# Kernel tuning notes

Measured on AMD Instinct MI355X. Metric: run time of the kernel, lower is better.

Reference implementation:

```python
import jax, jax.numpy as jnp
import numpy as np

H = 25  # fixed state size per module source
N_STEPS = 10


def _lstm_cell(x, h, c, W_ih, W_hh, b_ih, b_hh):
    # PyTorch LSTMCell: gates ordered i, f, g, o
    gates = x @ W_ih.T + b_ih + h @ W_hh.T + b_hh  # [B, 4H]
    i, f, g, o = jnp.split(gates, 4, axis=-1)
    c_new = jax.nn.sigmoid(f) * c + jax.nn.sigmoid(i) * jnp.tanh(g)
    h_new = jax.nn.sigmoid(o) * jnp.tanh(c_new)
    return h_new, c_new


def setup_inputs() -> dict:
    key = jax.random.key(0)
    ks = jax.random.split(key, 11)
    B, A = 131072, 18

    def u(k, shape, fan_in, fan_out):
        bound = np.sqrt(6.0 / (fan_in + fan_out)).astype(np.float32)
        return jax.random.uniform(k, shape, jnp.float32, -bound, bound)

    state = jax.random.normal(ks[0], (B, H), jnp.float32)
    # LSTMCell weights [4H, H]; biases zeroed per module init
    W_ih_enc = u(ks[1], (4 * H, H), H, 4 * H)
    W_hh_enc = u(ks[2], (4 * H, H), H, 4 * H)
    b_ih_enc = jnp.zeros((4 * H,), jnp.float32)
    b_hh_enc = jnp.zeros((4 * H,), jnp.float32)
    W_ih_dec = u(ks[3], (4 * H, H), H, 4 * H)
    W_hh_dec = u(ks[4], (4 * H, H), H, 4 * H)
    b_ih_dec = jnp.zeros((4 * H,), jnp.float32)
    b_hh_dec = jnp.zeros((4 * H,), jnp.float32)
    # actor head: norm_col_init std=0.01, bias 0
    w = jax.random.normal(ks[5], (A, H), jnp.float32)
    W_act = w * (0.01 / jnp.sqrt((w ** 2).sum(1, keepdims=True)))
    b_act = jnp.zeros((A,), jnp.float32)
    return {
        "state_repr_input": state,
        "W_ih_enc": W_ih_enc, "W_hh_enc": W_hh_enc, "b_ih_enc": b_ih_enc, "b_hh_enc": b_hh_enc,
        "W_ih_dec": W_ih_dec, "W_hh_dec": W_hh_dec, "b_ih_dec": b_ih_dec, "b_hh_dec": b_hh_dec,
        "W_act": W_act, "b_act": b_act,
    }


def reference(state_repr_input, W_ih_enc, W_hh_enc, b_ih_enc, b_hh_enc,
              W_ih_dec, W_hh_dec, b_ih_dec, b_hh_dec, W_act, b_act):
    B = state_repr_input.shape[0]
    zeros = jnp.zeros_like(state_repr_input)

    # Encoder: input to each step is previous hx (first step: state)
    def enc_step(carry, _):
        inp, h, c = carry
        h, c = _lstm_cell(inp, h, c, W_ih_enc, W_hh_enc, b_ih_enc, b_hh_enc)
        return (h, h, c), h

    (_, _, _), enc_hs = jax.lax.scan(enc_step, (state_repr_input, zeros, zeros), None, length=N_STEPS)
    # enc_hs: [10, B, 25]

    # Decoder: consumes encoder outputs in order
    def dec_step(carry, x):
        h, c = carry
        h, c = _lstm_cell(x, h, c, W_ih_dec, W_hh_dec, b_ih_dec, b_hh_dec)
        return (h, c), None

    (hx_dec, _), _ = jax.lax.scan(dec_step, (zeros, zeros), enc_hs)

    actor_lang = hx_dec @ W_act.T + b_act  # [B, A]
    return actor_lang, enc_hs
```

## Files before the change

kernel.cpp:

```cpp
#include <hip/hip_runtime.h>


#define HH 25
#define NSTEP 10
#define AOUT 18
#define WPB 8
#define BLK (WPB * 64)
#define NFRG 26
#define FPAD 40
#define LOG2E 1.44269504088896340736f

typedef __attribute__((ext_vector_type(8))) short short8;
typedef __attribute__((ext_vector_type(4))) float f32x4;

__device__ __forceinline__ short f2bf(float x) {
    unsigned u = __float_as_uint(x);
    u += 0x7fffu + ((u >> 16) & 1u);
    return (short)(u >> 16);
}
__device__ __forceinline__ unsigned cvtpk(float lo, float hi) {
    unsigned r;
    asm("v_cvt_pk_bf16_f32 %0, %1, %2" : "=v"(r) : "v"(lo), "v"(hi));
    return r;
}
#if __has_builtin(__builtin_amdgcn_exp2f)
#define EXP2(x) __builtin_amdgcn_exp2f(x)
#else
#define EXP2(x) exp2f(x)
#endif
#define RCP(x) __builtin_amdgcn_rcpf(x)
#define MFMA16(a, b, c) __builtin_amdgcn_mfma_f32_16x16x32_bf16((a), (b), (c), 0, 0, 0)

__global__ __launch_bounds__(BLK, 4)
void langnn_mfma16(const float* __restrict__ state,
                   const float* __restrict__ Wih_e, const float* __restrict__ Whh_e,
                   const float* __restrict__ bih_e, const float* __restrict__ bhh_e,
                   const float* __restrict__ Wih_d, const float* __restrict__ Whh_d,
                   const float* __restrict__ bih_d, const float* __restrict__ bhh_d,
                   const float* __restrict__ Wact, const float* __restrict__ bact,
                   float* __restrict__ out, int B)
{
    __shared__ __align__(16) short sFrag[NFRG][64][8];
    __shared__ __align__(16) short sH[2][WPB][16][FPAD];

    const int tid  = threadIdx.x;
    const int lane = tid & 63;
    const int w    = tid >> 6;
    const int r    = lane & 15;
    const int g    = lane >> 4;

    for (int i = tid; i < NFRG * 64; i += BLK) {
        const int idx = i >> 6, l = i & 63;
        const int lj = l & 15, lg = l >> 4;
        const float *W1 = nullptr, *W2 = nullptr, *B1 = nullptr, *B2 = nullptr;
        int gt = 0, jt, jmax = HH;
        if (idx < 8)       { gt = idx >> 1;        jt = idx & 1; W1 = Wih_e; W2 = Whh_e; B1 = bih_e; B2 = bhh_e; }
        else if (idx < 16) { gt = (idx - 8) >> 1;  jt = idx & 1; W1 = Wih_d; B1 = bih_d; B2 = bhh_d; }
        else if (idx < 24) { gt = (idx - 16) >> 1; jt = idx & 1; W1 = Whh_d; }
        else               { jt = idx - 24;        W1 = Wact;    B1 = bact;  jmax = AOUT; }
        const bool actor = (idx >= 24);
        const float sc = actor ? 1.f : (gt == 2 ? 2.f * LOG2E : -LOG2E);
        const int col = jt * 16 + lj;
        const int nrow = actor ? col : gt * HH + col;
        for (int e = 0; e < 8; ++e) {
            const int k = lg * 8 + e;
            float v = 0.f;
            if (col < jmax) {
                if (k < HH) {
                    v = W1[nrow * HH + k];
                    if (W2) v += W2[nrow * HH + k];
                    v *= sc;
                } else if (k == HH && B1) {
                    v = B1[nrow];
                    if (B2) v += B2[nrow];
                    v *= sc;
                }
            }
            sFrag[idx][l][e] = f2bf(v);
        }
    }
    {
        short* W0 = &sH[1][0][0][0];
        for (int i = tid; i < 8 * 64; i += BLK) {
            const int idx = i >> 6, l = i & 63;
            const int lj = l & 15, lg = l >> 4;
            const int gt = idx >> 1, jt = idx & 1;
            const float sc = (gt == 2 ? 2.f * LOG2E : -LOG2E);
            const int col = jt * 16 + lj;
            const int nrow = gt * HH + col;
            for (int e = 0; e < 8; ++e) {
                const int k = lg * 8 + e;
                float v = 0.f;
                if (col < HH) {
                    if (k < HH)       v = Wih_e[nrow * HH + k] * sc;
                    else if (k == HH) v = (bih_e[nrow] + bhh_e[nrow]) * sc;
                }
                W0[(size_t)idx * 512 + l * 8 + e] = f2bf(v);
            }
        }
    }
    {
        int* z = (int*)&sH[0][0][0][0];
        for (int i = tid; i < WPB * 16 * (FPAD / 2); i += BLK)
            z[i] = ((i % (FPAD / 2)) == 12) ? 0x3F800000 : 0;
    }
    __syncthreads();

    const int b0 = (blockIdx.x * WPB + w) * 16;
    float* pe = out + (size_t)B * AOUT + (size_t)(b0 + g * 4) * HH + r;

    float ce[2][4], cd[2][4];
    #pragma unroll
    for (int jt = 0; jt < 2; ++jt)
        #pragma unroll
        for (int q = 0; q < 4; ++q) { ce[jt][q] = 0.f; cd[jt][q] = 0.f; }

    short8 aE, aD;
    {
        const float* sp0 = state + (size_t)(b0 + r) * HH;
        #pragma unroll
        for (int e = 0; e < 8; ++e) {
            const int k = g * 8 + e;
            aE[e] = (k < HH) ? f2bf(sp0[k]) : (k == HH ? (short)0x3F80 : (short)0);
            aD[e] = (k == HH) ? (short)0x3F80 : (short)0;
        }
    }

    auto encCell = [&](const short (*FB)[64][8]) {
        #pragma unroll
        for (int jt = 0; jt < 2; ++jt) {
            f32x4 acc[4];
            #pragma unroll
            for (int gt = 0; gt < 4; ++gt) {
                short8 Bf = *(const short8*)&FB[gt * 2 + jt][lane][0];
                f32x4 z; z[0] = z[1] = z[2] = z[3] = 0.f;
                acc[gt] = MFMA16(aE, Bf, z);
            }
            float hv[4];
            #pragma unroll
            for (int q = 0; q < 4; ++q) {
                float Ei = EXP2(acc[0][q]);
                float Ef = EXP2(acc[1][q]);
                float Eg = EXP2(acc[2][q]);
                float Eo = EXP2(acc[3][q]);
                float Pf = 1.f + Ef;
                float Pig = (1.f + Ei) * (1.f + Eg);
                float c = fmaf(ce[jt][q], Pig, (Eg - 1.f) * Pf) * RCP(Pf * Pig);
                ce[jt][q] = c;
                float Ec = EXP2(2.f * LOG2E * c);
                float Pc = 1.f + Ec;
                hv[q] = (Pc - 2.f) * RCP(Pc * (1.f + Eo));
            }
            if (jt == 0 || r < 9) {
                float* p = pe + jt * 16;
                p[0] = hv[0]; p[HH] = hv[1]; p[2 * HH] = hv[2]; p[3 * HH] = hv[3];
                unsigned p01 = cvtpk(hv[0], hv[1]), p23 = cvtpk(hv[2], hv[3]);
                short* sp = &sH[0][w][g * 4][jt * 16 + r];
                sp[0]        = (short)p01;
                sp[FPAD]     = (short)(p01 >> 16);
                sp[2 * FPAD] = (short)p23;
                sp[3 * FPAD] = (short)(p23 >> 16);
            }
        }
        aE = *(const short8*)&sH[0][w][r][g * 8];
        pe += (size_t)B * HH;
    };

    auto decCell = [&]() {
        #pragma unroll
        for (int jt = 0; jt < 2; ++jt) {
            f32x4 acc[4];
            #pragma unroll
            for (int gt = 0; gt < 4; ++gt) {
                short8 Bx = *(const short8*)&sFrag[8 + gt * 2 + jt][lane][0];
                short8 Bh = *(const short8*)&sFrag[16 + gt * 2 + jt][lane][0];
                f32x4 z; z[0] = z[1] = z[2] = z[3] = 0.f;
                acc[gt] = MFMA16(aD, Bh, MFMA16(aE, Bx, z));
            }
            float hv[4];
            #pragma unroll
            for (int q = 0; q < 4; ++q) {
                float Ei = EXP2(acc[0][q]);
                float Ef = EXP2(acc[1][q]);
                float Eg = EXP2(acc[2][q]);
                float Eo = EXP2(acc[3][q]);
                float Pf = 1.f + Ef;
                float Pig = (1.f + Ei) * (1.f + Eg);
                float c = fmaf(cd[jt][q], Pig, (Eg - 1.f) * Pf) * RCP(Pf * Pig);
                cd[jt][q] = c;
                float Ec = EXP2(2.f * LOG2E * c);
                float Pc = 1.f + Ec;
                hv[q] = (Pc - 2.f) * RCP(Pc * (1.f + Eo));
            }
            if (jt == 0 || r < 9) {
                unsigned p01 = cvtpk(hv[0], hv[1]), p23 = cvtpk(hv[2], hv[3]);
                short* sp = &sH[1][w][g * 4][jt * 16 + r];
                sp[0]        = (short)p01;
                sp[FPAD]     = (short)(p01 >> 16);
                sp[2 * FPAD] = (short)p23;
                sp[3 * FPAD] = (short)(p23 >> 16);
            }
        }
        aD = *(const short8*)&sH[1][w][r][g * 8];
    };

    encCell((const short (*)[64][8])&sH[1][0][0][0]);
    __syncthreads();
    {
        int* z = (int*)&sH[1][w][0][0];
        for (int i = lane; i < 16 * (FPAD / 2); i += 64)
            z[i] = ((i % (FPAD / 2)) == 12) ? 0x3F800000 : 0;
    }
    decCell();
    #pragma unroll 1
    for (int t = 1; t < NSTEP; ++t) {
        encCell(sFrag);
        decCell();
    }

    #pragma unroll
    for (int jt = 0; jt < 2; ++jt) {
        short8 Bf = *(const short8*)&sFrag[24 + jt][lane][0];
        f32x4 z; z[0] = z[1] = z[2] = z[3] = 0.f;
        f32x4 o = MFMA16(aD, Bf, z);
        if (jt == 0 || r < 2) {
            float* p = out + (size_t)(b0 + g * 4) * AOUT + jt * 16 + r;
            p[0] = o[0]; p[AOUT] = o[1]; p[2 * AOUT] = o[2]; p[3 * AOUT] = o[3];
        }
    }
}

extern "C" void kernel_launch(void* const* d_in, const int* in_sizes, int n_in,
                              void* d_out, int out_size, void* d_ws, size_t ws_size,
                              hipStream_t stream) {
    const float* state = (const float*)d_in[0];
    const float* Wih_e = (const float*)d_in[1];
    const float* Whh_e = (const float*)d_in[2];
    const float* bih_e = (const float*)d_in[3];
    const float* bhh_e = (const float*)d_in[4];
    const float* Wih_d = (const float*)d_in[5];
    const float* Whh_d = (const float*)d_in[6];
    const float* bih_d = (const float*)d_in[7];
    const float* bhh_d = (const float*)d_in[8];
    const float* Wact  = (const float*)d_in[9];
    const float* bact  = (const float*)d_in[10];

    int B = in_sizes[0] / HH;
    int grid = B / (WPB * 16);

    hipLaunchKernelGGL(langnn_mfma16, dim3(grid), dim3(BLK), 0, stream,
                       state, Wih_e, Whh_e, bih_e, bhh_e,
                       Wih_d, Whh_d, bih_d, bhh_d, Wact, bact,
                       (float*)d_out, B);
}
```

Baseline: 95.77 us.

## Skew encoder and decoder steps into one loop, halve waves per block

Restructures the recurrence so each loop iteration runs decoder step t together with encoder step t+1. Their MFMAs and activation math are independent, so they can interleave and hide latency. The first encoder step now builds its input-weight fragments in registers, which removes the shared-memory staging, a block barrier and a per-wave re-zero. Waves per block drop from 8 to 4, giving smaller blocks, but the fused loop raises register pressure and could reduce occupancy.

```diff
diff --git a/kernel.cpp b/kernel.cpp
--- a/kernel.cpp
+++ b/kernel.cpp
@@ -4,7 +4,7 @@
 #define HH 25
 #define NSTEP 10
 #define AOUT 18
-#define WPB 8
+#define WPB 4
 #define BLK (WPB * 64)
 #define NFRG 26
 #define FPAD 40
@@ -30,6 +30,21 @@
 #endif
 #define RCP(x) __builtin_amdgcn_rcpf(x)
 #define MFMA16(a, b, c) __builtin_amdgcn_mfma_f32_16x16x32_bf16((a), (b), (c), 0, 0, 0)
+
+#define ACT_ELEM(A0, A1, A2, A3, CREF, HOUT)                                   \
+    {                                                                          \
+        float Ei = EXP2(A0);                                                   \
+        float Ef = EXP2(A1);                                                   \
+        float Eg = EXP2(A2);                                                   \
+        float Eo = EXP2(A3);                                                   \
+        float Pf = 1.f + Ef;                                                   \
+        float Pig = (1.f + Ei) * (1.f + Eg);                                   \
+        float c = fmaf(CREF, Pig, (Eg - 1.f) * Pf) * RCP(Pf * Pig);            \
+        CREF = c;                                                              \
+        float Ec = EXP2(2.f * LOG2E * c);                                      \
+        float Pc = 1.f + Ec;                                                   \
+        HOUT = (Pc - 2.f) * RCP(Pc * (1.f + Eo));                              \
+    }
 
 __global__ __launch_bounds__(BLK, 4)
 void langnn_mfma16(const float* __restrict__ state,
@@ -80,28 +95,8 @@
         }
     }
     {
-        short* W0 = &sH[1][0][0][0];
-        for (int i = tid; i < 8 * 64; i += BLK) {
-            const int idx = i >> 6, l = i & 63;
-            const int lj = l & 15, lg = l >> 4;
-            const int gt = idx >> 1, jt = idx & 1;
-            const float sc = (gt == 2 ? 2.f * LOG2E : -LOG2E);
-            const int col = jt * 16 + lj;
-            const int nrow = gt * HH + col;
-            for (int e = 0; e < 8; ++e) {
-                const int k = lg * 8 + e;
-                float v = 0.f;
-                if (col < HH) {
-                    if (k < HH)       v = Wih_e[nrow * HH + k] * sc;
-                    else if (k == HH) v = (bih_e[nrow] + bhh_e[nrow]) * sc;
-                }
-                W0[(size_t)idx * 512 + l * 8 + e] = f2bf(v);
-            }
-        }
-    }
-    {
-        int* z = (int*)&sH[0][0][0][0];
-        for (int i = tid; i < WPB * 16 * (FPAD / 2); i += BLK)
+        int* z = (int*)sH;
+        for (int i = tid; i < 2 * WPB * 16 * (FPAD / 2); i += BLK)
             z[i] = ((i % (FPAD / 2)) == 12) ? 0x3F800000 : 0;
     }
     __syncthreads();
@@ -126,31 +121,40 @@
         }
     }
 
-    auto encCell = [&](const short (*FB)[64][8]) {
+    {
+        short8 W0f[8];
+        #pragma unroll
+        for (int gt = 0; gt < 4; ++gt) {
+            const float sc = (gt == 2 ? 2.f * LOG2E : -LOG2E);
+            #pragma unroll
+            for (int jt = 0; jt < 2; ++jt) {
+                const int col = jt * 16 + r;
+                short8 v8;
+                #pragma unroll
+                for (int e = 0; e < 8; ++e) {
+                    const int k = g * 8 + e;
+                    float v = 0.f;
+                    if (col < HH) {
+                        if (k < HH)       v = Wih_e[(gt * HH + col) * HH + k] * sc;
+                        else if (k == HH) v = (bih_e[gt * HH + col] + bhh_e[gt * HH + col]) * sc;
+                    }
+                    v8[e] = f2bf(v);
+                }
+                W0f[gt * 2 + jt] = v8;
+            }
+        }
         #pragma unroll
         for (int jt = 0; jt < 2; ++jt) {
             f32x4 acc[4];
             #pragma unroll
             for (int gt = 0; gt < 4; ++gt) {
-                short8 Bf = *(const short8*)&FB[gt * 2 + jt][lane][0];
                 f32x4 z; z[0] = z[1] = z[2] = z[3] = 0.f;
-                acc[gt] = MFMA16(aE, Bf, z);
+                acc[gt] = MFMA16(aE, W0f[gt * 2 + jt], z);
             }
             float hv[4];
             #pragma unroll
-            for (int q = 0; q < 4; ++q) {
-                float Ei = EXP2(acc[0][q]);
-                float Ef = EXP2(acc[1][q]);
-                float Eg = EXP2(acc[2][q]);
-                float Eo = EXP2(acc[3][q]);
-                float Pf = 1.f + Ef;
-                float Pig = (1.f + Ei) * (1.f + Eg);
-                float c = fmaf(ce[jt][q], Pig, (Eg - 1.f) * Pf) * RCP(Pf * Pig);
-                ce[jt][q] = c;
-                float Ec = EXP2(2.f * LOG2E * c);
-                float Pc = 1.f + Ec;
-                hv[q] = (Pc - 2.f) * RCP(Pc * (1.f + Eo));
-            }
+            for (int q = 0; q < 4; ++q)
+                ACT_ELEM(acc[0][q], acc[1][q], acc[2][q], acc[3][q], ce[jt][q], hv[q]);
             if (jt == 0 || r < 9) {
                 float* p = pe + jt * 16;
                 p[0] = hv[0]; p[HH] = hv[1]; p[2 * HH] = hv[2]; p[3 * HH] = hv[3];
@@ -164,59 +168,74 @@
         }
         aE = *(const short8*)&sH[0][w][r][g * 8];
         pe += (size_t)B * HH;
-    };
-
-    auto decCell = [&]() {
+    }
+
+    #pragma unroll 1
+    for (int t = 0; t < NSTEP - 1; ++t) {
         #pragma unroll
         for (int jt = 0; jt < 2; ++jt) {
-            f32x4 acc[4];
+            f32x4 accD[4], accE[4];
             #pragma unroll
             for (int gt = 0; gt < 4; ++gt) {
                 short8 Bx = *(const short8*)&sFrag[8 + gt * 2 + jt][lane][0];
                 short8 Bh = *(const short8*)&sFrag[16 + gt * 2 + jt][lane][0];
+                short8 Be = *(const short8*)&sFrag[gt * 2 + jt][lane][0];
                 f32x4 z; z[0] = z[1] = z[2] = z[3] = 0.f;
-                acc[gt] = MFMA16(aD, Bh, MFMA16(aE, Bx, z));
-            }
-            float hv[4];
+                accD[gt] = MFMA16(aD, Bh, MFMA16(aE, Bx, z));
+                accE[gt] = MFMA16(aE, Be, z);
+            }
+            float hvD[4], hvE[4];
             #pragma unroll
             for (int q = 0; q < 4; ++q) {
-                float Ei = EXP2(acc[0][q]);
-                float Ef = EXP2(acc[1][q]);
-                float Eg = EXP2(acc[2][q]);
-                float Eo = EXP2(acc[3][q]);
-                float Pf = 1.f + Ef;
-                float Pig = (1.f + Ei) * (1.f + Eg);
-                float c = fmaf(cd[jt][q], Pig, (Eg - 1.f) * Pf) * RCP(Pf * Pig);
-                cd[jt][q] = c;
-                float Ec = EXP2(2.f * LOG2E * c);
-                float Pc = 1.f + Ec;
-                hv[q] = (Pc - 2.f) * RCP(Pc * (1.f + Eo));
+                ACT_ELEM(accD[0][q], accD[1][q], accD[2][q], accD[3][q], cd[jt][q], hvD[q]);
+                ACT_ELEM(accE[0][q], accE[1][q], accE[2][q], accE[3][q], ce[jt][q], hvE[q]);
             }
             if (jt == 0 || r < 9) {
-                unsigned p01 = cvtpk(hv[0], hv[1]), p23 = cvtpk(hv[2], hv[3]);
-                short* sp = &sH[1][w][g * 4][jt * 16 + r];
-                sp[0]        = (short)p01;
-                sp[FPAD]     = (short)(p01 >> 16);
-                sp[2 * FPAD] = (short)p23;
-                sp[3 * FPAD] = (short)(p23 >> 16);
-            }
-        }
+                float* p = pe + jt * 16;
+                p[0] = hvE[0]; p[HH] = hvE[1]; p[2 * HH] = hvE[2]; p[3 * HH] = hvE[3];
+                unsigned d01 = cvtpk(hvD[0], hvD[1]), d23 = cvtpk(hvD[2], hvD[3]);
+                unsigned e01 = cvtpk(hvE[0], hvE[1]), e23 = cvtpk(hvE[2], hvE[3]);
+                short* spD = &sH[1][w][g * 4][jt * 16 + r];
+                short* spE = &sH[0][w][g * 4][jt * 16 + r];
+                spD[0]        = (short)d01;
+                spD[FPAD]     = (short)(d01 >> 16);
+                spD[2 * FPAD] = (short)d23;
+                spD[3 * FPAD] = (short)(d23 >> 16);
+                spE[0]        = (short)e01;
+                spE[FPAD]     = (short)(e01 >> 16);
+                spE[2 * FPAD] = (short)e23;
+                spE[3 * FPAD] = (short)(e23 >> 16);
+            }
+        }
+        aE = *(const short8*)&sH[0][w][r][g * 8];
         aD = *(const short8*)&sH[1][w][r][g * 8];
-    };
-
-    encCell((const short (*)[64][8])&sH[1][0][0][0]);
-    __syncthreads();
-    {
-        int* z = (int*)&sH[1][w][0][0];
-        for (int i = lane; i < 16 * (FPAD / 2); i += 64)
-            z[i] = ((i % (FPAD / 2)) == 12) ? 0x3F800000 : 0;
-    }
-    decCell();
-    #pragma unroll 1
-    for (int t = 1; t < NSTEP; ++t) {
-        encCell(sFrag);
-        decCell();
-    }
+        pe += (size_t)B * HH;
+    }
+
+    #pragma unroll
+    for (int jt = 0; jt < 2; ++jt) {
+        f32x4 acc[4];
+        #pragma unroll
+        for (int gt = 0; gt < 4; ++gt) {
+            short8 Bx = *(const short8*)&sFrag[8 + gt * 2 + jt][lane][0];
+            short8 Bh = *(const short8*)&sFrag[16 + gt * 2 + jt][lane][0];
+            f32x4 z; z[0] = z[1] = z[2] = z[3] = 0.f;
+            acc[gt] = MFMA16(aD, Bh, MFMA16(aE, Bx, z));
+        }
+        float hv[4];
+        #pragma unroll
+        for (int q = 0; q < 4; ++q)
+            ACT_ELEM(acc[0][q], acc[1][q], acc[2][q], acc[3][q], cd[jt][q], hv[q]);
+        if (jt == 0 || r < 9) {
+            unsigned p01 = cvtpk(hv[0], hv[1]), p23 = cvtpk(hv[2], hv[3]);
+            short* sp = &sH[1][w][g * 4][jt * 16 + r];
+            sp[0]        = (short)p01;
+            sp[FPAD]     = (short)(p01 >> 16);
+            sp[2 * FPAD] = (short)p23;
+            sp[3 * FPAD] = (short)(p23 >> 16);
+        }
+    }
+    aD = *(const short8*)&sH[1][w][r][g * 8];
 
     #pragma unroll
     for (int jt = 0; jt < 2; ++jt) {
```

Measured after the change: 115.1 us. 20.2% more time.
